# Optimization experiments

Hardware: AMD Instinct MI355X
Metric: run time of the kernel (lower is better)

The kernel has to match this reference:

```python
import jax, jax.numpy as jnp
import numpy as np

N = 100000   # nodes
E = 1000000  # edges
IN, HID, OUT = 128, 64, 64


def setup_inputs() -> dict:
    key = jax.random.key(0)
    ks = jax.random.split(key, 6)
    x = jax.random.normal(ks[0], (N, IN), dtype=jnp.float32)
    edge_index = jax.random.randint(ks[1], (2, E), 0, N, dtype=jnp.int64)
    edge_attr = jax.random.uniform(ks[2], (E,), dtype=jnp.float32)
    # Glorot-style init like PyG GCNConv (weight [in, out], bias zeros)
    W1 = jax.random.normal(ks[3], (IN, HID), dtype=jnp.float32) * (1.0 / np.sqrt(IN))
    b1 = jnp.zeros((HID,), dtype=jnp.float32)
    W2 = jax.random.normal(ks[4], (HID, OUT), dtype=jnp.float32) * (1.0 / np.sqrt(HID))
    b2 = jnp.zeros((OUT,), dtype=jnp.float32)
    return {"x": x, "edge_index": edge_index, "edge_attr": edge_attr,
            "W1": W1, "b1": b1, "W2": W2, "b2": b2}


def gcn_conv(x, edge_index, edge_weight, W, b):
    """GCNConv: add self-loops, symmetric normalization, linear + scatter-add."""
    n = x.shape[0]
    row, col = edge_index[0], edge_index[1]
    loop = jnp.arange(n, dtype=row.dtype)
    row = jnp.concatenate([row, loop])
    col = jnp.concatenate([col, loop])
    w = jnp.concatenate([edge_weight, jnp.ones((n,), dtype=x.dtype)])
    deg = jax.ops.segment_sum(w, col, num_segments=n)              # [N]
    dinv = jnp.where(deg > 0, jax.lax.rsqrt(deg), 0.0)
    norm = dinv[row] * w * dinv[col]                               # [E+N]
    h = x @ W                                                      # [N, out]
    agg = jax.ops.segment_sum(h[row] * norm[:, None], col, num_segments=n)
    return agg + b


def reference(x, edge_index, edge_attr, W1, b1, W2, b2):
    h = jax.nn.relu(gcn_conv(x, edge_index, edge_attr, W1, b1))
    return jax.nn.relu(gcn_conv(h, edge_index, edge_attr, W2, b2))
```

## Files before the change

kernel.cpp:

```cpp
#include <hip/hip_runtime.h>


#define BNODES 512
#define LB 9
#define MAXBKT 256
#define EPT 12
#define EPB (256 * EPT)

typedef __attribute__((ext_vector_type(8))) short bf16x8;
typedef __attribute__((ext_vector_type(8))) unsigned short u16x8;
typedef __attribute__((ext_vector_type(8))) float f32x8;
typedef __attribute__((ext_vector_type(4))) float f32x4;

__device__ __forceinline__ unsigned short f2bf(float f) {
    unsigned u = __float_as_uint(f);
    u = (u + 0x7FFF + ((u >> 16) & 1)) >> 16;
    return (unsigned short)u;
}
__device__ __forceinline__ float bf2f(unsigned short h) {
    return __uint_as_float(((unsigned)h) << 16);
}
__device__ __forceinline__ f32x8 bf8tof(u16x8 u) {
    f32x8 r;
    #pragma unroll
    for (int i = 0; i < 8; ++i) r[i] = bf2f(u[i]);
    return r;
}

__device__ __forceinline__ int waveIncScan(int v, int lane) {
    #pragma unroll
    for (int d = 1; d < 64; d <<= 1) {
        int u = __shfl_up(v, d, 64);
        if (lane >= d) v += u;
    }
    return v;
}

template<int NW>
__device__ __forceinline__ int blockIncScan(int v, int t, int* wt) {
    int lane = t & 63, w = t >> 6;
    int s = waveIncScan(v, lane);
    if (lane == 63) wt[w] = s;
    __syncthreads();
    int add = 0;
    #pragma unroll
    for (int i = 0; i < NW - 1; ++i) if (i < w) add += wt[i];
    return s + add;
}

__device__ __forceinline__ f32x8 gather8(
    const unsigned short* __restrict__ G, const int2* __restrict__ sedge,
    int s, int m, int p8, f32x8 a0)
{
    f32x8 a1 = (f32x8)0.f;
    int e = s, e_end = s + m;
    if ((((unsigned long long)(sedge + e)) & 8) && e < e_end) {
        int2 pk = sedge[e++];
        float w = __int_as_float(pk.y);
        a0 += w * bf8tof(*(const u16x8*)&G[(size_t)pk.x * 64 + p8 * 8]);
    }
    for (; e + 1 < e_end; e += 2) {
        int4 pp = *(const int4*)&sedge[e];
        float w0 = __int_as_float(pp.y);
        float w1 = __int_as_float(pp.w);
        u16x8 g0 = *(const u16x8*)&G[(size_t)pp.x * 64 + p8 * 8];
        u16x8 g1 = *(const u16x8*)&G[(size_t)pp.z * 64 + p8 * 8];
        a0 += w0 * bf8tof(g0);
        a1 += w1 * bf8tof(g1);
    }
    if (e < e_end) {
        int2 pk = sedge[e];
        float w = __int_as_float(pk.y);
        a0 += w * bf8tof(*(const u16x8*)&G[(size_t)pk.x * 64 + p8 * 8]);
    }
    return a0 + a1;
}


__global__ __launch_bounds__(256) void hist_kernel(
    const int* __restrict__ col, int* __restrict__ H, int E, int NBKT,
    const float* __restrict__ W1, const float* __restrict__ W2,
    unsigned short* __restrict__ WT1, unsigned short* __restrict__ WT2, int NEB)
{
    int t = threadIdx.x, blk = blockIdx.x;
    if (blk >= NEB) {
        int i = (blk - NEB) * 256 + t;
        if (i < 64 * 128) {
            int c = i >> 7, k = i & 127;
            WT1[i] = f2bf(W1[k * 64 + c]);
        } else if (i < 64 * 128 + 64 * 64) {
            int j = i - 64 * 128;
            int c = j >> 6, k = j & 63;
            WT2[j] = f2bf(W2[k * 64 + c]);
        }
        return;
    }
    __shared__ int h[MAXBKT];
    for (int b = t; b < NBKT; b += 256) h[b] = 0;
    __syncthreads();
    int base = blk * EPB;
    #pragma unroll
    for (int i = 0; i < EPT; ++i) {
        int e = base + i * 256 + t;
        if (e < E) atomicAdd(&h[col[e] >> LB], 1);
    }
    __syncthreads();
    for (int b = t; b < NBKT; b += 256) H[blk * NBKT + b] = h[b];
}

__global__ __launch_bounds__(512) void rowscan_kernel(
    int* __restrict__ H, int* __restrict__ rowSum, int NEB, int NBKT)
{
    __shared__ int wt[8];
    int b = blockIdx.x, t = threadIdx.x;
    int v = (t < NEB) ? H[t * NBKT + b] : 0;
    int incl = blockIncScan<8>(v, t, wt);
    if (t < NEB) H[t * NBKT + b] = incl - v;
    if (t == 511) rowSum[b] = incl;
}

__global__ __launch_bounds__(256) void scatter_gemm_kernel(
    const int* __restrict__ row, const int* __restrict__ col,
    const float* __restrict__ w, const int* __restrict__ H,
    const int* __restrict__ rowSum, int2* __restrict__ sedge1,
    int E, int NBKT, int NEB,
    const float* __restrict__ X, const unsigned short* __restrict__ WT,
    unsigned short* __restrict__ G, int n)
{
    __shared__ __align__(16) char smem[32768];
    const int t = threadIdx.x;
    const int blk = blockIdx.x;

    if (blk < NEB) {
        int2* stage = (int2*)smem;
        unsigned char* bstage = (unsigned char*)(stage + EPB);
        int* lcnt  = (int*)(bstage + EPB);
        int* loff  = lcnt + MAXBKT;
        int* lcur  = loff + MAXBKT;
        int* gbase = lcur + MAXBKT;
        int* wt    = gbase + MAXBKT;

        int vb = (t < NBKT) ? rowSum[t] : 0;
        int ib = blockIncScan<4>(vb, t, wt);
        if (t < NBKT) gbase[t] = (ib - vb) + H[blk * NBKT + t];
        for (int b = t; b < NBKT; b += 256) lcnt[b] = 0;
        __syncthreads();

        int base = blk * EPB;
        #pragma unroll
        for (int i = 0; i < EPT; ++i) {
            int e = base + i * 256 + t;
            if (e < E) atomicAdd(&lcnt[col[e] >> LB], 1);
        }
        __syncthreads();
        int v = (t < NBKT) ? lcnt[t] : 0;
        int incl = blockIncScan<4>(v, t, wt);
        if (t < NBKT) {
            int x0 = incl - v;
            loff[t] = x0;
            lcur[t] = x0;
        }
        __syncthreads();
        #pragma unroll
        for (int i = 0; i < EPT; ++i) {
            int e = base + i * 256 + t;
            if (e < E) {
                int c = col[e];
                int b = c >> LB;
                int pos = atomicAdd(&lcur[b], 1);
                int2 pk;
                pk.x = row[e] | ((c & (BNODES - 1)) << 20);
                pk.y = __float_as_int(w[e]);
                stage[pos] = pk;
                bstage[pos] = (unsigned char)b;
            }
        }
        __syncthreads();
        int ecnt = E - base; if (ecnt > EPB) ecnt = EPB;
        for (int i = t; i < ecnt; i += 256) {
            int b = bstage[i];
            int g = gbase[b] + (i - loff[b]);
            sedge1[g] = stage[i];
        }
        return;
    }

    constexpr int K = 128, ROWB = 256, SLOTS = 16, CPR = 32;
    char* xs = smem;
    char* ws = smem + 64 * ROWB;
    const int nodeBase = (blk - NEB) * 64;

    for (int q = t; q < 64 * SLOTS; q += 256) {
        int r = q / SLOTS, s = q % SLOTS;
        uint4 v = *(const uint4*)(WT + r * K + s * 8);
        *(uint4*)(ws + r * ROWB + ((s ^ (r & 7)) * 16)) = v;
    }
    for (int q = t; q < 64 * CPR; q += 256) {
        int r = q / CPR, c = q % CPR;
        int node = nodeBase + r;
        float4 v = make_float4(0.f, 0.f, 0.f, 0.f);
        if (node < n) v = *(const float4*)(X + (size_t)node * K + c * 4);
        ushort4 h;
        h.x = f2bf(v.x); h.y = f2bf(v.y); h.z = f2bf(v.z); h.w = f2bf(v.w);
        *(ushort4*)(xs + r * ROWB + (((c >> 1) ^ (r & 7)) * 16) + (c & 1) * 8) = h;
    }
    __syncthreads();

    const int lane = t & 63;
    const int wv = t >> 6;
    const int lr = lane & 15;
    const int lk = lane >> 4;
    const int arow = (wv << 4) + lr;

    f32x4 acc[4] = {};
    #pragma unroll
    for (int kb = 0; kb < 4; ++kb) {
        int s = kb * 4 + lk;
        bf16x8 a = *(bf16x8*)(xs + arow * ROWB + ((s ^ (arow & 7)) * 16));
        #pragma unroll
        for (int cb = 0; cb < 4; ++cb) {
            int c = cb * 16 + lr;
            bf16x8 b = *(bf16x8*)(ws + c * ROWB + ((s ^ (c & 7)) * 16));
            acc[cb] = __builtin_amdgcn_mfma_f32_16x16x32_bf16(a, b, acc[cb], 0, 0, 0);
        }
    }

    int rowbase = nodeBase + (wv << 4) + (lk << 2);
    #pragma unroll
    for (int j = 0; j < 4; ++j) {
        int node = rowbase + j;
        if (node >= n) continue;
        #pragma unroll
        for (int cb = 0; cb < 4; ++cb)
            G[(size_t)node * 64 + cb * 16 + lr] = f2bf(acc[cb][j]);
    }
}

__global__ __launch_bounds__(512) void fine_kernel(
    const int2* __restrict__ sedge1, const int* __restrict__ rowSum,
    int2* __restrict__ sedge2, int* __restrict__ nodeStart,
    int* __restrict__ nodeCnt, float* __restrict__ dinv,
    unsigned short* __restrict__ g1, int n, int NBKT)
{
    __shared__ int cnt[BNODES];
    __shared__ float wsum[BNODES];
    __shared__ int off[BNODES];
    __shared__ int cur[BNODES];
    __shared__ float dloc[BNODES];
    __shared__ int bs[MAXBKT + 1];
    __shared__ int wt[8];
    int b = blockIdx.x, t = threadIdx.x;

    int vb = (t < NBKT) ? rowSum[t] : 0;
    int ib = blockIncScan<8>(vb, t, wt);
    if (t < NBKT) bs[t] = ib - vb;
    if (t == 511) bs[NBKT] = ib;
    cnt[t] = 0; wsum[t] = 1.0f;
    __syncthreads();

    int s = bs[b], e = (b + 1 <= NBKT) ? bs[b + 1] : bs[NBKT];
    for (int j = s + t; j < e; j += 512) {
        int2 pk = sedge1[j];
        int ld = pk.x >> 20;
        atomicAdd(&cnt[ld], 1);
        atomicAdd(&wsum[ld], __int_as_float(pk.y));
    }
    __syncthreads();
    int v = cnt[t];
    int incl = blockIncScan<8>(v, t, wt);
    int x0 = s + incl - v;
    off[t] = x0;
    cur[t] = x0;
    dloc[t] = rsqrtf(wsum[t]);
    __syncthreads();
    int node = b * BNODES + t;
    if (node < n) {
        nodeStart[node] = off[t];
        nodeCnt[node] = cnt[t];
        dinv[node] = dloc[t];
    }
    for (int j = s + t; j < e; j += 512) {
        int2 pk = sedge1[j];
        int ld = pk.x >> 20;
        int pos = atomicAdd(&cur[ld], 1);
        sedge2[pos] = make_int2(pk.x & 0xFFFFF, pk.y);
    }
    for (int q = t; q < BNODES * 8; q += 512) {
        int r = q >> 3, cc = q & 7;
        int nd = b * BNODES + r;
        if (nd >= n) continue;
        float dv = dloc[r];
        size_t offb = (size_t)nd * 64 + cc * 8;
        ushort4 u0 = *(const ushort4*)(g1 + offb);
        ushort4 u1 = *(const ushort4*)(g1 + offb + 4);
        u0.x = f2bf(bf2f(u0.x) * dv); u0.y = f2bf(bf2f(u0.y) * dv);
        u0.z = f2bf(bf2f(u0.z) * dv); u0.w = f2bf(bf2f(u0.w) * dv);
        u1.x = f2bf(bf2f(u1.x) * dv); u1.y = f2bf(bf2f(u1.y) * dv);
        u1.z = f2bf(bf2f(u1.z) * dv); u1.w = f2bf(bf2f(u1.w) * dv);
        *(ushort4*)(g1 + offb) = u0;
        *(ushort4*)(g1 + offb + 4) = u1;
    }
}

__global__ __launch_bounds__(256) void aggmm_kernel(
    const unsigned short* __restrict__ G1, const int2* __restrict__ sedge2,
    const int* __restrict__ nodeStart, const int* __restrict__ nodeCnt,
    const float* __restrict__ dinv, const float* __restrict__ bias,
    const unsigned short* __restrict__ WT2, unsigned short* __restrict__ G2, int n)
{
    constexpr int BN = 32;
    constexpr int ROWB = 128;
    __shared__ char smem[(BN + 64) * ROWB];
    char* xs = smem;
    char* ws = smem + BN * ROWB;
    const int tid = threadIdx.x;
    const int nodeBase = blockIdx.x * BN;

    for (int q = tid; q < 64 * 8; q += 256) {
        int r = q >> 3, s = q & 7;
        uint4 v = *(const uint4*)(WT2 + r * 64 + s * 8);
        *(uint4*)(ws + r * ROWB + ((s ^ (r & 7)) * 16)) = v;
    }

    int p8 = tid & 7;
    int r = tid >> 3;
    int node = nodeBase + r;
    f32x8 o = (f32x8)0.f;
    if (node < n) {
        f32x8 a = bf8tof(*(const u16x8*)&G1[(size_t)node * 64 + p8 * 8]);
        a = gather8(G1, sedge2, nodeStart[node], nodeCnt[node], p8, a);
        float di = dinv[node];
        #pragma unroll
        for (int i = 0; i < 8; ++i)
            o[i] = fmaxf(fmaf(di, a[i], bias[p8 * 8 + i]), 0.f);
    }
    u16x8 h;
    #pragma unroll
    for (int i = 0; i < 8; ++i) h[i] = f2bf(o[i]);
    *(u16x8*)(xs + r * ROWB + ((p8 ^ (r & 7)) * 16)) = h;
    __syncthreads();

    const int lane = tid & 63;
    const int w = tid >> 6;
    const int lr = lane & 15;
    const int lk = lane >> 4;
    const int rb = w >> 1;
    const int arow = rb * 16 + lr;

    f32x4 acc[2] = {};
    #pragma unroll
    for (int kb = 0; kb < 2; ++kb) {
        int s = kb * 4 + lk;
        bf16x8 a = *(bf16x8*)(xs + arow * ROWB + ((s ^ (arow & 7)) * 16));
        #pragma unroll
        for (int cc = 0; cc < 2; ++cc) {
            int c = ((w & 1) * 2 + cc) * 16 + lr;
            bf16x8 b = *(bf16x8*)(ws + c * ROWB + ((s ^ (c & 7)) * 16));
            acc[cc] = __builtin_amdgcn_mfma_f32_16x16x32_bf16(a, b, acc[cc], 0, 0, 0);
        }
    }

    int rowbase = nodeBase + rb * 16 + (lk << 2);
    #pragma unroll
    for (int j = 0; j < 4; ++j) {
        int nd = rowbase + j;
        if (nd >= n) continue;
        float dv = dinv[nd];
        #pragma unroll
        for (int cc = 0; cc < 2; ++cc)
            G2[(size_t)nd * 64 + ((w & 1) * 2 + cc) * 16 + lr] = f2bf(acc[cc][j] * dv);
    }
}

__global__ __launch_bounds__(256) void agg_kernel(
    const unsigned short* __restrict__ G, const int2* __restrict__ sedge2,
    const int* __restrict__ nodeStart, const int* __restrict__ nodeCnt,
    const float* __restrict__ dinv, const float* __restrict__ bias,
    float* __restrict__ OUT, int n)
{
    int t = blockIdx.x * blockDim.x + threadIdx.x;
    if (t >= n * 8) return;
    int node = t >> 3, p8 = t & 7;

    f32x8 a = bf8tof(*(const u16x8*)&G[(size_t)node * 64 + p8 * 8]);
    a = gather8(G, sedge2, nodeStart[node], nodeCnt[node], p8, a);

    float di = dinv[node];
    float4 o0, o1;
    o0.x = fmaxf(fmaf(di, a[0], bias[p8 * 8 + 0]), 0.f);
    o0.y = fmaxf(fmaf(di, a[1], bias[p8 * 8 + 1]), 0.f);
    o0.z = fmaxf(fmaf(di, a[2], bias[p8 * 8 + 2]), 0.f);
    o0.w = fmaxf(fmaf(di, a[3], bias[p8 * 8 + 3]), 0.f);
    o1.x = fmaxf(fmaf(di, a[4], bias[p8 * 8 + 4]), 0.f);
    o1.y = fmaxf(fmaf(di, a[5], bias[p8 * 8 + 5]), 0.f);
    o1.z = fmaxf(fmaf(di, a[6], bias[p8 * 8 + 6]), 0.f);
    o1.w = fmaxf(fmaf(di, a[7], bias[p8 * 8 + 7]), 0.f);
    *(float4*)&OUT[(size_t)node * 64 + p8 * 8] = o0;
    *(float4*)&OUT[(size_t)node * 64 + p8 * 8 + 4] = o1;
}

extern "C" void kernel_launch(void* const* d_in, const int* in_sizes, int n_in,
                              void* d_out, int out_size, void* d_ws, size_t ws_size,
                              hipStream_t stream) {
    const float* x     = (const float*)d_in[0];
    const int*   eidx  = (const int*)d_in[1];
    const float* eattr = (const float*)d_in[2];
    const float* W1    = (const float*)d_in[3];
    const float* b1    = (const float*)d_in[4];
    const float* W2    = (const float*)d_in[5];
    const float* b2    = (const float*)d_in[6];
    float* out = (float*)d_out;

    const int n = in_sizes[0] / 128;
    const int E = in_sizes[2];
    const int* row = eidx;
    const int* col = eidx + E;

    const int NBKT = (n + BNODES - 1) / BNODES;
    const int NEB  = (E + EPB - 1) / EPB;

    int2*  sedge1 = (int2*)d_ws;
    int2*  sedge2 = sedge1 + (size_t)E;
    unsigned short* g1 = (unsigned short*)(sedge2 + (size_t)E);
    unsigned short* g2 = g1 + (size_t)n * 64;
    unsigned short* WT1 = g2 + (size_t)n * 64;
    unsigned short* WT2 = WT1 + 64 * 128;
    float* dinv      = (float*)(WT2 + 64 * 64);
    int*   nodeStart = (int*)(dinv + n);
    int*   nodeCnt   = nodeStart + n;
    int*   H         = nodeCnt + n;
    int*   rowSum    = H + (size_t)NEB * NBKT;

    const int nbG  = (n + 63) / 64;
    const int nbG2 = (n + 31) / 32;
    const int nbA8 = (int)(((size_t)n * 8 + 255) / 256);

    hist_kernel<<<NEB + 48, 256, 0, stream>>>(col, H, E, NBKT, W1, W2, WT1, WT2, NEB);
    rowscan_kernel<<<NBKT, 512, 0, stream>>>(H, rowSum, NEB, NBKT);
    scatter_gemm_kernel<<<NEB + nbG, 256, 0, stream>>>(
        row, col, eattr, H, rowSum, sedge1, E, NBKT, NEB, x, WT1, g1, n);
    fine_kernel<<<NBKT, 512, 0, stream>>>(sedge1, rowSum, sedge2, nodeStart,
                                          nodeCnt, dinv, g1, n, NBKT);

    aggmm_kernel<<<nbG2, 256, 0, stream>>>(g1, sedge2, nodeStart, nodeCnt, dinv, b1, WT2, g2, n);
    agg_kernel<<<nbA8, 256, 0, stream>>>(g2, sedge2, nodeStart, nodeCnt, dinv, b2, out, n);
}
```

Measured before the change: 108.9 us.

## Fold symmetric normalization into per-edge weights and split fine kernel

Splits the fine kernel into two launches: one computes degrees, dinv and CSR offsets, and the other builds the sorted edge list with each edge weight pre-multiplied by dinv[row]*dinv[col]. This drops the in-place rescale pass over g1 and the per-node dinv multiplies in the aggregation and GEMM epilogues; the self-loop term now uses di*di. The cost is an extra kernel launch, a second read of sedge1, and a random gather of dinv[row] per edge.

```diff
diff --git a/kernel.cpp b/kernel.cpp
--- a/kernel.cpp
+++ b/kernel.cpp
@@ -236,15 +236,48 @@
     }
 }
 
-__global__ __launch_bounds__(512) void fine_kernel(
+__global__ __launch_bounds__(512) void fine_dinv_kernel(
     const int2* __restrict__ sedge1, const int* __restrict__ rowSum,
-    int2* __restrict__ sedge2, int* __restrict__ nodeStart,
-    int* __restrict__ nodeCnt, float* __restrict__ dinv,
-    unsigned short* __restrict__ g1, int n, int NBKT)
+    int* __restrict__ nodeStart, int* __restrict__ nodeCnt,
+    float* __restrict__ dinv, int n, int NBKT)
 {
     __shared__ int cnt[BNODES];
     __shared__ float wsum[BNODES];
-    __shared__ int off[BNODES];
+    __shared__ int bs[MAXBKT + 1];
+    __shared__ int wt[8];
+    int b = blockIdx.x, t = threadIdx.x;
+
+    int vb = (t < NBKT) ? rowSum[t] : 0;
+    int ib = blockIncScan<8>(vb, t, wt);
+    if (t < NBKT) bs[t] = ib - vb;
+    if (t == 511) bs[NBKT] = ib;
+    cnt[t] = 0; wsum[t] = 1.0f;
+    __syncthreads();
+
+    int s = bs[b], e = bs[b + 1];
+    for (int j = s + t; j < e; j += 512) {
+        int2 pk = sedge1[j];
+        int ld = pk.x >> 20;
+        atomicAdd(&cnt[ld], 1);
+        atomicAdd(&wsum[ld], __int_as_float(pk.y));
+    }
+    __syncthreads();
+    int v = cnt[t];
+    int incl = blockIncScan<8>(v, t, wt);
+    int x0 = s + incl - v;
+    int node = b * BNODES + t;
+    if (node < n) {
+        nodeStart[node] = x0;
+        nodeCnt[node] = v;
+        dinv[node] = rsqrtf(wsum[t]);
+    }
+}
+
+__global__ __launch_bounds__(512) void fine_csr_kernel(
+    const int2* __restrict__ sedge1, const int* __restrict__ rowSum,
+    const int* __restrict__ nodeStart, const float* __restrict__ dinv,
+    int2* __restrict__ sedge2, int n, int NBKT)
+{
     __shared__ int cur[BNODES];
     __shared__ float dloc[BNODES];
     __shared__ int bs[MAXBKT + 1];
@@ -255,50 +288,19 @@
     int ib = blockIncScan<8>(vb, t, wt);
     if (t < NBKT) bs[t] = ib - vb;
     if (t == 511) bs[NBKT] = ib;
-    cnt[t] = 0; wsum[t] = 1.0f;
-    __syncthreads();
-
-    int s = bs[b], e = (b + 1 <= NBKT) ? bs[b + 1] : bs[NBKT];
+    int node = b * BNODES + t;
+    cur[t]  = (node < n) ? nodeStart[node] : 0;
+    dloc[t] = (node < n) ? dinv[node] : 0.f;
+    __syncthreads();
+
+    int s = bs[b], e = bs[b + 1];
     for (int j = s + t; j < e; j += 512) {
         int2 pk = sedge1[j];
         int ld = pk.x >> 20;
-        atomicAdd(&cnt[ld], 1);
-        atomicAdd(&wsum[ld], __int_as_float(pk.y));
-    }
-    __syncthreads();
-    int v = cnt[t];
-    int incl = blockIncScan<8>(v, t, wt);
-    int x0 = s + incl - v;
-    off[t] = x0;
-    cur[t] = x0;
-    dloc[t] = rsqrtf(wsum[t]);
-    __syncthreads();
-    int node = b * BNODES + t;
-    if (node < n) {
-        nodeStart[node] = off[t];
-        nodeCnt[node] = cnt[t];
-        dinv[node] = dloc[t];
-    }
-    for (int j = s + t; j < e; j += 512) {
-        int2 pk = sedge1[j];
-        int ld = pk.x >> 20;
+        int rw = pk.x & 0xFFFFF;
         int pos = atomicAdd(&cur[ld], 1);
-        sedge2[pos] = make_int2(pk.x & 0xFFFFF, pk.y);
-    }
-    for (int q = t; q < BNODES * 8; q += 512) {
-        int r = q >> 3, cc = q & 7;
-        int nd = b * BNODES + r;
-        if (nd >= n) continue;
-        float dv = dloc[r];
-        size_t offb = (size_t)nd * 64 + cc * 8;
-        ushort4 u0 = *(const ushort4*)(g1 + offb);
-        ushort4 u1 = *(const ushort4*)(g1 + offb + 4);
-        u0.x = f2bf(bf2f(u0.x) * dv); u0.y = f2bf(bf2f(u0.y) * dv);
-        u0.z = f2bf(bf2f(u0.z) * dv); u0.w = f2bf(bf2f(u0.w) * dv);
-        u1.x = f2bf(bf2f(u1.x) * dv); u1.y = f2bf(bf2f(u1.y) * dv);
-        u1.z = f2bf(bf2f(u1.z) * dv); u1.w = f2bf(bf2f(u1.w) * dv);
-        *(ushort4*)(g1 + offb) = u0;
-        *(ushort4*)(g1 + offb + 4) = u1;
+        float wp = __int_as_float(pk.y) * dinv[rw] * dloc[ld];
+        sedge2[pos] = make_int2(rw, __float_as_int(wp));
     }
 }
 
@@ -327,12 +329,12 @@
     int node = nodeBase + r;
     f32x8 o = (f32x8)0.f;
     if (node < n) {
-        f32x8 a = bf8tof(*(const u16x8*)&G1[(size_t)node * 64 + p8 * 8]);
+        float di = dinv[node];
+        f32x8 a = (di * di) * bf8tof(*(const u16x8*)&G1[(size_t)node * 64 + p8 * 8]);
         a = gather8(G1, sedge2, nodeStart[node], nodeCnt[node], p8, a);
-        float di = dinv[node];
         #pragma unroll
         for (int i = 0; i < 8; ++i)
-            o[i] = fmaxf(fmaf(di, a[i], bias[p8 * 8 + i]), 0.f);
+            o[i] = fmaxf(a[i] + bias[p8 * 8 + i], 0.f);
     }
     u16x8 h;
     #pragma unroll
@@ -365,10 +367,9 @@
     for (int j = 0; j < 4; ++j) {
         int nd = rowbase + j;
         if (nd >= n) continue;
-        float dv = dinv[nd];
         #pragma unroll
         for (int cc = 0; cc < 2; ++cc)
-            G2[(size_t)nd * 64 + ((w & 1) * 2 + cc) * 16 + lr] = f2bf(acc[cc][j] * dv);
+            G2[(size_t)nd * 64 + ((w & 1) * 2 + cc) * 16 + lr] = f2bf(acc[cc][j]);
     }
 }
 
@@ -382,19 +383,19 @@
     if (t >= n * 8) return;
     int node = t >> 3, p8 = t & 7;
 
-    f32x8 a = bf8tof(*(const u16x8*)&G[(size_t)node * 64 + p8 * 8]);
+    float di = dinv[node];
+    f32x8 a = (di * di) * bf8tof(*(const u16x8*)&G[(size_t)node * 64 + p8 * 8]);
     a = gather8(G, sedge2, nodeStart[node], nodeCnt[node], p8, a);
 
-    float di = dinv[node];
     float4 o0, o1;
-    o0.x = fmaxf(fmaf(di, a[0], bias[p8 * 8 + 0]), 0.f);
-    o0.y = fmaxf(fmaf(di, a[1], bias[p8 * 8 + 1]), 0.f);
-    o0.z = fmaxf(fmaf(di, a[2], bias[p8 * 8 + 2]), 0.f);
-    o0.w = fmaxf(fmaf(di, a[3], bias[p8 * 8 + 3]), 0.f);
-    o1.x = fmaxf(fmaf(di, a[4], bias[p8 * 8 + 4]), 0.f);
-    o1.y = fmaxf(fmaf(di, a[5], bias[p8 * 8 + 5]), 0.f);
-    o1.z = fmaxf(fmaf(di, a[6], bias[p8 * 8 + 6]), 0.f);
-    o1.w = fmaxf(fmaf(di, a[7], bias[p8 * 8 + 7]), 0.f);
+    o0.x = fmaxf(a[0] + bias[p8 * 8 + 0], 0.f);
+    o0.y = fmaxf(a[1] + bias[p8 * 8 + 1], 0.f);
+    o0.z = fmaxf(a[2] + bias[p8 * 8 + 2], 0.f);
+    o0.w = fmaxf(a[3] + bias[p8 * 8 + 3], 0.f);
+    o1.x = fmaxf(a[4] + bias[p8 * 8 + 4], 0.f);
+    o1.y = fmaxf(a[5] + bias[p8 * 8 + 5], 0.f);
+    o1.z = fmaxf(a[6] + bias[p8 * 8 + 6], 0.f);
+    o1.w = fmaxf(a[7] + bias[p8 * 8 + 7], 0.f);
     *(float4*)&OUT[(size_t)node * 64 + p8 * 8] = o0;
     *(float4*)&OUT[(size_t)node * 64 + p8 * 8 + 4] = o1;
 }
@@ -439,8 +440,10 @@
     rowscan_kernel<<<NBKT, 512, 0, stream>>>(H, rowSum, NEB, NBKT);
     scatter_gemm_kernel<<<NEB + nbG, 256, 0, stream>>>(
         row, col, eattr, H, rowSum, sedge1, E, NBKT, NEB, x, WT1, g1, n);
-    fine_kernel<<<NBKT, 512, 0, stream>>>(sedge1, rowSum, sedge2, nodeStart,
-                                          nodeCnt, dinv, g1, n, NBKT);
+    fine_dinv_kernel<<<NBKT, 512, 0, stream>>>(sedge1, rowSum, nodeStart, nodeCnt,
+                                               dinv, n, NBKT);
+    fine_csr_kernel<<<NBKT, 512, 0, stream>>>(sedge1, rowSum, nodeStart, dinv,
+                                              sedge2, n, NBKT);
 
     aggmm_kernel<<<nbG2, 256, 0, stream>>>(g1, sedge2, nodeStart, nodeCnt, dinv, b1, WT2, g2, n);
     agg_kernel<<<nbA8, 256, 0, stream>>>(g2, sedge2, nodeStart, nodeCnt, dinv, b2, out, n);
```

Result: no change. 109.0 us, median of 2 (+0.2%).
